# Kernel tuning notes

Measured on AMD Instinct MI355X. Metric: run time of the kernel, lower is better.

Reference implementation:

```python
import jax, jax.numpy as jnp
import numpy as np

B, T, E, H = 2, 1024, 1024, 16
D = E // H
HEAVY_RATIO = 0.1
RECENT_RATIO = 0.1
QUANT_RATIO = 0.5  # module-level global `quantized_ratio`
NEG = jnp.finfo(jnp.float32).min


def setup_inputs() -> dict:
    key = jax.random.key(0)
    ks = jax.random.split(key, 10)
    s = 0.02
    hidden_states = jax.random.normal(ks[0], (B, T, E), jnp.float32)
    causal = jnp.tril(jnp.ones((T, T), bool))
    attention_mask = jnp.broadcast_to(jnp.where(causal, 0.0, NEG).astype(jnp.float32)[None, None], (B, 1, T, T))
    lin = lambda k: (jax.random.normal(k, (E, E), jnp.float32) * s)
    return {
        'hidden_states': hidden_states,
        'attention_mask': attention_mask,
        'Wq': lin(ks[1]), 'bq': jnp.zeros((E,), jnp.float32),
        'Wk': lin(ks[2]), 'bk': jnp.zeros((E,), jnp.float32),
        'Wv': lin(ks[3]), 'bv': jnp.zeros((E,), jnp.float32),
        'Wo': lin(ks[4]), 'bo': jnp.zeros((E,), jnp.float32),
    }


def _heavy_hitter_mask(aw, hb):
    # aw: [BH, T, T] masked attn logits. Faithful to local_heavy_hitter_mask
    # (use_gumbel=False path, no padding). Returns bool mask_bottom [BH, T, T].
    BH, Tt, _ = aw.shape
    tmp = jax.nn.softmax(aw, axis=-1)               # fp32 softmax
    acc = tmp[:, :hb, :].sum(axis=1)                # [BH, T]
    acc = acc * (jnp.arange(Tt) < hb)               # zero cols >= hb
    col_lt_hb = (jnp.arange(Tt) < hb)
    init_block = jnp.broadcast_to(col_lt_hb[None, None, :], (BH, hb, Tt))
    row_ids = jnp.arange(BH)[:, None]
    cols = jnp.arange(Tt)

    def step(acc, xs):
        row, t = xs                                  # row: [BH, T], t: scalar index
        tmp_i = jax.nn.softmax(row, axis=-1)
        _, idx = jax.lax.top_k(acc, hb - 1)          # heavy-hitter indices [BH, hb-1]
        mb = jnp.zeros((BH, Tt), bool).at[row_ids, idx].set(True)
        mb = mb | (cols == t)[None, :]               # always keep current token
        acc = (acc + tmp_i) * mb                     # accumulate + evict
        return acc, mb

    ts = jnp.arange(hb, Tt)
    rows = jnp.swapaxes(aw[:, hb:, :], 0, 1)         # [T-hb, BH, T]
    _, mbs = jax.lax.scan(step, acc, (rows, ts))
    mask = jnp.concatenate([init_block, jnp.swapaxes(mbs, 0, 1)], axis=1)
    return jnp.tril(mask)


def reference(hidden_states, attention_mask, Wq, bq, Wk, bk, Wv, bv, Wo, bo):
    scaling = D ** -0.5
    shape = lambda x: jnp.transpose(x.reshape(B, T, H, D), (0, 2, 1, 3)).reshape(B * H, T, D)
    q = shape((hidden_states @ Wq + bq) * scaling)
    k = shape(hidden_states @ Wk + bk)
    v = shape(hidden_states @ Wv + bv)

    aw = jnp.einsum('btd,bsd->bts', q, k)                      # [BH, T, T]
    aw = aw.reshape(B, H, T, T) + attention_mask               # additive causal mask
    aw = jnp.maximum(aw, NEG).reshape(B * H, T, T)

    hb = int(HEAVY_RATIO * T)
    qt = int(hb * QUANT_RATIO)
    hb = hb + qt                                               # inflated heavy budget
    recent = int(RECENT_RATIO * T)

    mask_bottom = _heavy_hitter_mask(jax.lax.stop_gradient(aw), hb)
    recent_mask = jnp.triu(jnp.ones((T, T), bool), -recent)    # recent window
    mask = jnp.tril(mask_bottom | recent_mask[None])

    # torch code recomputes the identical masked logits; reuse aw
    aw = jnp.where(mask, aw, jnp.min(attention_mask))
    probs = jax.nn.softmax(aw, axis=-1)
    out = jnp.einsum('bts,bsd->btd', probs, v)                 # [BH, T, D]
    out = jnp.transpose(out.reshape(B, H, T, D), (0, 2, 1, 3)).reshape(B, T, E)
    return out @ Wo + bo
```

## Files before the change

### kernel.cpp

```cpp
#include <hip/hip_runtime.h>
#include <hip/hip_bf16.h>
#include <stdint.h>

#define TT 1024
#define EE 1024
#define HH 16
#define DD 64
#define BHN 32
#define HB 153
#define RECW 102
#define RING 16
#define INFLT 8
#define NEGF (-3.4028234663852886e38f)

typedef unsigned long long ull;
typedef __attribute__((ext_vector_type(8))) short bf16x8;
typedef __attribute__((ext_vector_type(4))) float f32x4;

#define OFF_Q  ((size_t)0)
#define OFF_K  (OFF_Q + (size_t)BHN*TT*DD)
#define OFF_V  (OFF_K + (size_t)BHN*TT*DD)
#define OFF_AW (OFF_V + (size_t)BHN*TT*DD)
#define OFF_M  (OFF_AW + (size_t)BHN*TT*TT)
#define OFF_S  (OFF_M + (size_t)BHN*TT)
#define OFF_AO (OFF_S + (size_t)BHN*TT)
#define OFF_END (OFF_AO + (size_t)BHN*TT*DD)

__device__ __forceinline__ ushort f2bf(float x) {
  unsigned u = __float_as_uint(x);
  u = (u + 0x7FFF + ((u >> 16) & 1)) >> 16;
  return (ushort)u;
}
__device__ __forceinline__ float bf2f(ushort h) {
  return __uint_as_float((unsigned)h << 16);
}

__global__ __launch_bounds__(256) void k_pmm(const float* __restrict__ X,
    const float* __restrict__ W, const float* __restrict__ bias,
    float* __restrict__ Y, float scale, int mode) {
  __shared__ ushort Ah[64][72], Al[64][72];
  __shared__ ushort Bh[64][72], Bl[64][72];
  int tid = threadIdx.x, lane = tid & 63, wid = tid >> 6;
  int r = tid >> 2, c0 = (tid & 3) * 16;
  int r0 = blockIdx.y * 64, n0 = blockIdx.x * 64;

  f32x4 acc[4];
  #pragma unroll
  for (int nc = 0; nc < 4; ++nc) acc[nc] = (f32x4){0.f, 0.f, 0.f, 0.f};

  for (int k0 = 0; k0 < EE; k0 += 64) {
    __syncthreads();
    {
      const float4* xs = (const float4*)(X + (size_t)(r0 + r) * EE + k0 + c0);
      #pragma unroll
      for (int q4 = 0; q4 < 4; ++q4) {
        float4 v = xs[q4];
        float f[4] = {v.x, v.y, v.z, v.w};
        ushort hi[4], lo[4];
        #pragma unroll
        for (int u = 0; u < 4; ++u) {
          hi[u] = f2bf(f[u]);
          lo[u] = f2bf(f[u] - bf2f(hi[u]));
        }
        *(unsigned*)&Ah[r][c0 + q4*4]     = (unsigned)hi[0] | ((unsigned)hi[1] << 16);
        *(unsigned*)&Ah[r][c0 + q4*4 + 2] = (unsigned)hi[2] | ((unsigned)hi[3] << 16);
        *(unsigned*)&Al[r][c0 + q4*4]     = (unsigned)lo[0] | ((unsigned)lo[1] << 16);
        *(unsigned*)&Al[r][c0 + q4*4 + 2] = (unsigned)lo[2] | ((unsigned)lo[3] << 16);
      }
    }
    {
      const float4* wsrc = (const float4*)(W + (size_t)(k0 + r) * EE + n0 + c0);
      #pragma unroll
      for (int q4 = 0; q4 < 4; ++q4) {
        float4 v = wsrc[q4];
        float f[4] = {v.x, v.y, v.z, v.w};
        #pragma unroll
        for (int u = 0; u < 4; ++u) {
          ushort hi = f2bf(f[u]);
          ushort lo = f2bf(f[u] - bf2f(hi));
          int c = c0 + q4*4 + u;
          Bh[c][r] = hi;
          Bl[c][r] = lo;
        }
      }
    }
    __syncthreads();
    #pragma unroll
    for (int kb = 0; kb < 2; ++kb) {
      bf16x8 ah = *(const bf16x8*)&Ah[wid*16 + (lane & 15)][kb*32 + (lane >> 4)*8];
      bf16x8 al = *(const bf16x8*)&Al[wid*16 + (lane & 15)][kb*32 + (lane >> 4)*8];
      #pragma unroll
      for (int nc = 0; nc < 4; ++nc) {
        bf16x8 bh_ = *(const bf16x8*)&Bh[nc*16 + (lane & 15)][kb*32 + (lane >> 4)*8];
        bf16x8 bl_ = *(const bf16x8*)&Bl[nc*16 + (lane & 15)][kb*32 + (lane >> 4)*8];
        acc[nc] = __builtin_amdgcn_mfma_f32_16x16x32_bf16(ah, bh_, acc[nc], 0, 0, 0);
        acc[nc] = __builtin_amdgcn_mfma_f32_16x16x32_bf16(al, bh_, acc[nc], 0, 0, 0);
        acc[nc] = __builtin_amdgcn_mfma_f32_16x16x32_bf16(ah, bl_, acc[nc], 0, 0, 0);
      }
    }
  }

  int rowbase = wid*16 + (lane >> 4)*4;
  #pragma unroll
  for (int nc = 0; nc < 4; ++nc) {
    int c = n0 + nc*16 + (lane & 15);
    float bv = bias[c];
    #pragma unroll
    for (int qq = 0; qq < 4; ++qq) {
      int rr = r0 + rowbase + qq;
      float val = (acc[nc][qq] + bv) * scale;
      int b_ = rr >> 10, t_ = rr & 1023, h_ = c >> 6, d_ = c & 63;
      if (mode == 1) {
        Y[(((size_t)(b_*HH + h_) * TT) + t_) * DD + d_] = val;
      } else if (mode == 2) {
        ((ushort*)Y)[(((size_t)(b_*HH + h_) * TT) + t_) * DD + d_] = f2bf(val);
      } else {
        Y[(size_t)rr * EE + c] = val;
      }
    }
  }
}

__global__ __launch_bounds__(256) void k_qk_mfma(const float* __restrict__ q,
    const float* __restrict__ k, float* __restrict__ aw) {
  int bh = blockIdx.y, tt = blockIdx.x;
  int t0 = tt * 64;
  int tid = threadIdx.x, lane = tid & 63, wid = tid >> 6;
  int r = tid >> 2, c0 = (tid & 3) * 16;
  __shared__ ushort Qh[64][72], Ql[64][72];
  __shared__ ushort Kh[64][72], Kl[64][72];
  const float* qb = q + (size_t)bh * TT * DD;
  const float* kb = k + (size_t)bh * TT * DD;
  float* awb = aw + (size_t)bh * TT * TT;

  {
    const float4* xs = (const float4*)(qb + (size_t)(t0 + r) * DD + c0);
    #pragma unroll
    for (int q4 = 0; q4 < 4; ++q4) {
      float4 v = xs[q4];
      float f[4] = {v.x, v.y, v.z, v.w};
      ushort hi[4], lo[4];
      #pragma unroll
      for (int u = 0; u < 4; ++u) {
        hi[u] = f2bf(f[u]);
        lo[u] = f2bf(f[u] - bf2f(hi[u]));
      }
      *(unsigned*)&Qh[r][c0 + q4*4]     = (unsigned)hi[0] | ((unsigned)hi[1] << 16);
      *(unsigned*)&Qh[r][c0 + q4*4 + 2] = (unsigned)hi[2] | ((unsigned)hi[3] << 16);
      *(unsigned*)&Ql[r][c0 + q4*4]     = (unsigned)lo[0] | ((unsigned)lo[1] << 16);
      *(unsigned*)&Ql[r][c0 + q4*4 + 2] = (unsigned)lo[2] | ((unsigned)lo[3] << 16);
    }
  }

  for (int st = 0; st <= tt; ++st) {
    __syncthreads();
    {
      const float4* xs = (const float4*)(kb + (size_t)(st * 64 + r) * DD + c0);
      #pragma unroll
      for (int q4 = 0; q4 < 4; ++q4) {
        float4 v = xs[q4];
        float f[4] = {v.x, v.y, v.z, v.w};
        ushort hi[4], lo[4];
        #pragma unroll
        for (int u = 0; u < 4; ++u) {
          hi[u] = f2bf(f[u]);
          lo[u] = f2bf(f[u] - bf2f(hi[u]));
        }
        *(unsigned*)&Kh[r][c0 + q4*4]     = (unsigned)hi[0] | ((unsigned)hi[1] << 16);
        *(unsigned*)&Kh[r][c0 + q4*4 + 2] = (unsigned)hi[2] | ((unsigned)hi[3] << 16);
        *(unsigned*)&Kl[r][c0 + q4*4]     = (unsigned)lo[0] | ((unsigned)lo[1] << 16);
        *(unsigned*)&Kl[r][c0 + q4*4 + 2] = (unsigned)lo[2] | ((unsigned)lo[3] << 16);
      }
    }
    __syncthreads();
    f32x4 acc[4];
    #pragma unroll
    for (int nc = 0; nc < 4; ++nc) acc[nc] = (f32x4){0.f, 0.f, 0.f, 0.f};
    #pragma unroll
    for (int kb2 = 0; kb2 < 2; ++kb2) {
      bf16x8 ah = *(const bf16x8*)&Qh[wid*16 + (lane & 15)][kb2*32 + (lane >> 4)*8];
      bf16x8 al = *(const bf16x8*)&Ql[wid*16 + (lane & 15)][kb2*32 + (lane >> 4)*8];
      #pragma unroll
      for (int nc = 0; nc < 4; ++nc) {
        bf16x8 bh_ = *(const bf16x8*)&Kh[nc*16 + (lane & 15)][kb2*32 + (lane >> 4)*8];
        bf16x8 bl_ = *(const bf16x8*)&Kl[nc*16 + (lane & 15)][kb2*32 + (lane >> 4)*8];
        acc[nc] = __builtin_amdgcn_mfma_f32_16x16x32_bf16(ah, bh_, acc[nc], 0, 0, 0);
        acc[nc] = __builtin_amdgcn_mfma_f32_16x16x32_bf16(al, bh_, acc[nc], 0, 0, 0);
        acc[nc] = __builtin_amdgcn_mfma_f32_16x16x32_bf16(ah, bl_, acc[nc], 0, 0, 0);
      }
    }
    int rowbase = wid*16 + (lane >> 4)*4;
    #pragma unroll
    for (int nc = 0; nc < 4; ++nc) {
      int s = st * 64 + nc*16 + (lane & 15);
      #pragma unroll
      for (int qq = 0; qq < 4; ++qq) {
        int t_ = t0 + rowbase + qq;
        awb[(size_t)t_ * TT + s] = acc[nc][qq];
      }
    }
  }
}

__global__ __launch_bounds__(256) void k_softmax(float* __restrict__ aw) {
  int bh = blockIdx.y;
  int wid = threadIdx.x >> 6, lane = threadIdx.x & 63;
  int t = blockIdx.x * 4 + wid;
  float* row = aw + ((size_t)bh * TT + t) * TT;
  float vals[16];
  float m = NEGF;
  #pragma unroll
  for (int i = 0; i < 16; ++i) {
    int j = lane + 64*i;
    vals[i] = (j <= t) ? row[j] : NEGF;
    m = fmaxf(m, vals[i]);
  }
  for (int o = 32; o; o >>= 1) m = fmaxf(m, __shfl_xor(m, o));
  float s = 0.f;
  #pragma unroll
  for (int i = 0; i < 16; ++i) {
    int j = lane + 64*i;
    if (j <= t) { vals[i] = expf(vals[i] - m); s += vals[i]; }
  }
  for (int o = 32; o; o >>= 1) s += __shfl_xor(s, o);
  float inv = 1.0f / s;
  #pragma unroll
  for (int i = 0; i < 16; ++i) {
    int j = lane + 64*i;
    if (j <= t) row[j] = vals[i] * inv;
  }
}

__global__ __launch_bounds__(256) void k_init_acc(const float* __restrict__ p,
    float* __restrict__ initacc) {
  int bh = blockIdx.x;
  int c = threadIdx.x;
  float val = 0.f;
  if (c < HB) {
    const float* pb = p + (size_t)bh * TT * TT;
    for (int i = c; i < HB; ++i)
      val += pb[(size_t)i * TT + c];
  }
  initacc[(size_t)bh * 256 + c] = val;
}

#define DPP_HOP(ctrl)                                                        \
  {                                                                          \
    unsigned tt = (unsigned)__builtin_amdgcn_update_dpp(                     \
        (int)0xFFFFFFFFu, (int)x, (ctrl), 0xF, 0xF, false);                  \
    x = x < tt ? x : tt;                                                     \
  }
__device__ __forceinline__ unsigned wave_min_u32(unsigned x) {
  DPP_HOP(0x111)
  DPP_HOP(0x112)
  DPP_HOP(0x114)
  DPP_HOP(0x118)
  DPP_HOP(0x142)
  DPP_HOP(0x143)
  return (unsigned)__builtin_amdgcn_readlane((int)x, 63);
}

__device__ __forceinline__ void gload_lds16(const float* gsrc, float* ldst) {
  __builtin_amdgcn_global_load_lds(
      (const __attribute__((address_space(1))) unsigned int*)gsrc,
      (__attribute__((address_space(3))) unsigned int*)ldst,
      16, 0, 0);
}

__global__ __launch_bounds__(128) void k_scan(const float* __restrict__ p,
    const float* __restrict__ initacc, int* __restrict__ evict_g) {
  int bh = blockIdx.x;
  int tid = threadIdx.x;
  int lane = tid & 63;
  const float* pb = p + (size_t)bh * TT * TT;
  __shared__ float ring[RING][TT];
  __shared__ int ev[TT];
  __shared__ volatile int rdyf[RING];
  __shared__ volatile int donef;
  for (int i = tid; i < TT; i += 128) ev[i] = 0x7fffffff;
  if (tid < RING) rdyf[tid] = -1;
  if (tid == 0) donef = -1;
  __syncthreads();

  if (tid >= 64) {
    #pragma unroll
    for (int r = 0; r < INFLT; ++r) {
      const float* srcrow = pb + (size_t)(HB + r) * TT;
      float* slotbase = ring[(HB + r) & (RING - 1)];
      #pragma unroll
      for (int j = 0; j < 4; ++j)
        gload_lds16(srcrow + j * 256 + lane * 4, slotbase + j * 256);
    }
    for (int r = HB; r < TT; ++r) {
      asm volatile("s_waitcnt vmcnt(28)" ::: "memory");
      if (lane == 0) rdyf[r & (RING - 1)] = r;
      int rn = r + INFLT;
      if (rn - RING >= HB) {
        while (donef < rn - RING) { }
      }
      int rsrc = rn < TT ? rn : TT - 1;
      const float* srcrow = pb + (size_t)rsrc * TT;
      float* slotbase = ring[rn & (RING - 1)];
      #pragma unroll
      for (int j = 0; j < 4; ++j)
        gload_lds16(srcrow + j * 256 + lane * 4, slotbase + j * 256);
    }
  } else {
    bool act2 = lane < (HB - 128);
    int col0 = lane, col1 = 64 + lane, col2 = act2 ? (128 + lane) : 0;
    float sc0 = initacc[(size_t)bh * 256 + lane];
    float sc1 = initacc[(size_t)bh * 256 + 64 + lane];
    float sc2 = act2 ? initacc[(size_t)bh * 256 + 128 + lane] : 0.f;

    while (rdyf[HB & (RING - 1)] != HB) { }
    asm volatile("" ::: "memory");
    int fpeek = rdyf[(HB + 1) & (RING - 1)];
    float r0, r1, r2, rd;
    {
      const float* rb = ring[HB & (RING - 1)];
      r0 = rb[col0]; r1 = rb[col1]; r2 = rb[col2]; rd = rb[HB];
    }
    int cstar;
    {
      unsigned b0 = __float_as_uint(sc0);
      unsigned b1 = __float_as_uint(sc1);
      unsigned b2 = act2 ? __float_as_uint(sc2) : 0xFFFFFFFFu;
      unsigned mn = b0 < b1 ? b0 : b1; mn = mn < b2 ? mn : b2;
      unsigned mstar = wave_min_u32(mn);
      unsigned c0k = (b0 == mstar) ? (unsigned)(1023 - col0) : 0xFFFFFFFFu;
      unsigned c1k = (b1 == mstar) ? (unsigned)(1023 - col1) : 0xFFFFFFFFu;
      unsigned c2k = (act2 && b2 == mstar) ? (unsigned)(1023 - col2) : 0xFFFFFFFFu;
      unsigned cm = c0k < c1k ? c0k : c1k; cm = cm < c2k ? cm : c2k;
      cstar = 1023 - (int)wave_min_u32(cm);
    }

    for (int t = HB; t < TT; ++t) {
      if (col0 == cstar) { ev[col0] = t; col0 = t; sc0 = rd; } else sc0 += r0;
      if (col1 == cstar) { ev[col1] = t; col1 = t; sc1 = rd; } else sc1 += r1;
      if (act2) {
        if (col2 == cstar) { ev[col2] = t; col2 = t; sc2 = rd; } else sc2 += r2;
      }
      if (lane == 0) donef = t;
      if (t + 1 < TT) {
        int slot = (t + 1) & (RING - 1);
        if (fpeek != t + 1) {
          while (rdyf[slot] != t + 1) { }
        }
        asm volatile("" ::: "memory");
        fpeek = rdyf[(t + 2) & (RING - 1)];
        const float* rb = ring[slot];
        r0 = rb[col0]; r1 = rb[col1]; r2 = rb[col2]; rd = rb[t + 1];
        unsigned b0 = __float_as_uint(sc0);
        unsigned b1 = __float_as_uint(sc1);
        unsigned b2 = act2 ? __float_as_uint(sc2) : 0xFFFFFFFFu;
        unsigned mn = b0 < b1 ? b0 : b1; mn = mn < b2 ? mn : b2;
        unsigned mstar = wave_min_u32(mn);
        unsigned c0k = (b0 == mstar) ? (unsigned)(1023 - col0) : 0xFFFFFFFFu;
        unsigned c1k = (b1 == mstar) ? (unsigned)(1023 - col1) : 0xFFFFFFFFu;
        unsigned c2k = (act2 && b2 == mstar) ? (unsigned)(1023 - col2) : 0xFFFFFFFFu;
        unsigned cm = c0k < c1k ? c0k : c1k; cm = cm < c2k ? cm : c2k;
        cstar = 1023 - (int)wave_min_u32(cm);
      }
    }
  }

  __syncthreads();
  int4* dst4 = (int4*)(evict_g + (size_t)bh * TT);
  const int4* src4 = (const int4*)ev;
  for (int i = tid; i < TT/4; i += 128) dst4[i] = src4[i];
}

__global__ __launch_bounds__(256) void k_pv(const float* __restrict__ p,
    const int* __restrict__ evict_g, const ushort* __restrict__ vbf,
    float* __restrict__ ao) {
  int bh = blockIdx.y, tt = blockIdx.x;
  int tid = threadIdx.x, lane = tid & 63, wid = tid >> 6;
  int t0 = tt * 64;
  __shared__ ushort PA[64][72];
  __shared__ ushort VT[64][72];
  __shared__ float rowsum[64];
  __shared__ int et[TT];
  ((int4*)et)[tid] = ((const int4*)(evict_g + (size_t)bh * TT))[tid];
  if (tid < 64) rowsum[tid] = 0.f;
  const float* pb = p + ((size_t)bh * TT + t0) * TT;
  const ushort* vb = vbf + (size_t)bh * TT * DD;

  f32x4 acc[4];
  #pragma unroll
  for (int nc = 0; nc < 4; ++nc) acc[nc] = (f32x4){0.f, 0.f, 0.f, 0.f};

  int r = tid >> 2;
  int c0 = (tid & 3) * 16;
  int tg = t0 + r;
  __syncthreads();

  for (int st = 0; st <= tt; ++st) {
    const float* prow = pb + (size_t)r * TT + st * 64 + c0;
    float part = 0.f;
    ushort tmp16[16];
    #pragma unroll
    for (int q4 = 0; q4 < 4; ++q4) {
      float4 pv4 = *(const float4*)(prow + q4 * 4);
      float vals[4] = {pv4.x, pv4.y, pv4.z, pv4.w};
      #pragma unroll
      for (int u = 0; u < 4; ++u) {
        int j = st * 64 + c0 + q4 * 4 + u;
        bool allow = (j <= tg) && ((et[j] > tg) || (j + RECW >= tg));
        float mv = allow ? vals[u] : 0.f;
        part += mv;
        tmp16[q4 * 4 + u] = f2bf(mv);
      }
    }
    #pragma unroll
    for (int w2 = 0; w2 < 8; ++w2) {
      unsigned pk = (unsigned)tmp16[w2 * 2] | ((unsigned)tmp16[w2 * 2 + 1] << 16);
      *(unsigned*)&PA[r][c0 + w2 * 2] = pk;
    }
    part += __shfl_xor(part, 1);
    part += __shfl_xor(part, 2);
    if ((tid & 3) == 0) rowsum[r] += part;
    {
      const unsigned* vrow32 = (const unsigned*)(vb + (size_t)(st * 64 + r) * DD + c0);
      #pragma unroll
      for (int u = 0; u < 8; ++u) {
        unsigned vv = vrow32[u];
        VT[c0 + u * 2][r] = (ushort)(vv & 0xFFFF);
        VT[c0 + u * 2 + 1][r] = (ushort)(vv >> 16);
      }
    }
    __syncthreads();
    #pragma unroll
    for (int kb = 0; kb < 2; ++kb) {
      bf16x8 af = *(const bf16x8*)&PA[wid * 16 + (lane & 15)][kb * 32 + (lane >> 4) * 8];
      #pragma unroll
      for (int nc = 0; nc < 4; ++nc) {
        bf16x8 bfr = *(const bf16x8*)&VT[nc * 16 + (lane & 15)][kb * 32 + (lane >> 4) * 8];
        acc[nc] = __builtin_amdgcn_mfma_f32_16x16x32_bf16(af, bfr, acc[nc], 0, 0, 0);
      }
    }
    __syncthreads();
  }

  int b_ = bh >> 4, h_ = bh & 15;
  int rl = wid * 16 + (lane >> 4) * 4;
  #pragma unroll
  for (int nc = 0; nc < 4; ++nc) {
    int d = nc * 16 + (lane & 15);
    #pragma unroll
    for (int qq = 0; qq < 4; ++qq) {
      int rr = rl + qq;
      float outv = acc[nc][qq] / rowsum[rr];
      ao[((size_t)b_ * TT + (t0 + rr)) * EE + h_ * DD + d] = outv;
    }
  }
}

extern "C" void kernel_launch(void* const* d_in, const int* in_sizes, int n_in,
                              void* d_out, int out_size, void* d_ws, size_t ws_size,
                              hipStream_t stream) {
  const float* hs = (const float*)d_in[0];
  const float* Wq = (const float*)d_in[2];
  const float* bq = (const float*)d_in[3];
  const float* Wk = (const float*)d_in[4];
  const float* bk = (const float*)d_in[5];
  const float* Wv = (const float*)d_in[6];
  const float* bv = (const float*)d_in[7];
  const float* Wo = (const float*)d_in[8];
  const float* bo = (const float*)d_in[9];
  float* out = (float*)d_out;

  float* ws = (float*)d_ws;
  float* q  = ws + OFF_Q;
  float* k  = ws + OFF_K;
  float* v  = ws + OFF_V;
  float* aw = ws + OFF_AW;
  float* ao = ws + OFF_AO;
  float* initacc = ws + OFF_END;
  int* evict = (int*)(ws + OFF_END + (size_t)BHN * 256);

  dim3 gproj(16, 32);
  k_pmm<<<gproj, 256, 0, stream>>>(hs, Wq, bq, q, 0.125f, 1);
  k_pmm<<<gproj, 256, 0, stream>>>(hs, Wk, bk, k, 1.0f, 1);
  k_pmm<<<gproj, 256, 0, stream>>>(hs, Wv, bv, v, 1.0f, 2);

  dim3 gqk(16, BHN);
  k_qk_mfma<<<gqk, 256, 0, stream>>>(q, k, aw);

  dim3 grs(TT/4, BHN);
  k_softmax<<<grs, 256, 0, stream>>>(aw);

  k_init_acc<<<BHN, 256, 0, stream>>>(aw, initacc);

  k_scan<<<BHN, 128, 0, stream>>>(aw, initacc, evict);

  dim3 gpv(16, BHN);
  k_pv<<<gpv, 256, 0, stream>>>(aw, evict, (const ushort*)v, ao);

  dim3 gout(16, 32);
  k_pmm<<<gout, 256, 0, stream>>>(ao, Wo, bo, out, 1.0f, 0);
}
```

Before: 632.1 us.

## Merge scan producer and consumer waves into one self-prefetching wave

The heavy-hitter scan kernel previously ran a producer wave that streamed rows into an LDS ring and a consumer wave that spun on LDS ready/done flags. Both roles now live in one 64-thread wave. It issues async global-to-LDS loads several rows ahead, waits on vmcnt, and reads with inline ds_read, so all cross-wave spin-wait handshakes are gone. The risk is that the serial eviction loop now also carries load issue and the vmcnt/lgkmcnt waits, which may lengthen each step. Correctness also depends on the hand-tuned vmcnt count and on ordering between LDS writes and later ring reuse.

```diff
diff --git a/kernel.cpp b/kernel.cpp
--- a/kernel.cpp
+++ b/kernel.cpp
@@ -16,6 +16,7 @@
 typedef unsigned long long ull;
 typedef __attribute__((ext_vector_type(8))) short bf16x8;
 typedef __attribute__((ext_vector_type(4))) float f32x4;
+typedef __attribute__((address_space(3))) float lds_float;
 
 #define OFF_Q  ((size_t)0)
 #define OFF_K  (OFF_Q + (size_t)BHN*TT*DD)
@@ -267,37 +268,50 @@
       16, 0, 0);
 }
 
-__global__ __launch_bounds__(128) void k_scan(const float* __restrict__ p,
+__global__ __launch_bounds__(64) void k_scan(const float* __restrict__ p,
     const float* __restrict__ initacc, int* __restrict__ evict_g) {
   int bh = blockIdx.x;
-  int tid = threadIdx.x;
-  int lane = tid & 63;
+  int lane = threadIdx.x;
   const float* pb = p + (size_t)bh * TT * TT;
   __shared__ float ring[RING][TT];
   __shared__ int ev[TT];
-  __shared__ volatile int rdyf[RING];
-  __shared__ volatile int donef;
-  for (int i = tid; i < TT; i += 128) ev[i] = 0x7fffffff;
-  if (tid < RING) rdyf[tid] = -1;
-  if (tid == 0) donef = -1;
-  __syncthreads();
-
-  if (tid >= 64) {
-    #pragma unroll
-    for (int r = 0; r < INFLT; ++r) {
-      const float* srcrow = pb + (size_t)(HB + r) * TT;
-      float* slotbase = ring[(HB + r) & (RING - 1)];
-      #pragma unroll
-      for (int j = 0; j < 4; ++j)
-        gload_lds16(srcrow + j * 256 + lane * 4, slotbase + j * 256);
-    }
-    for (int r = HB; r < TT; ++r) {
-      asm volatile("s_waitcnt vmcnt(28)" ::: "memory");
-      if (lane == 0) rdyf[r & (RING - 1)] = r;
-      int rn = r + INFLT;
-      if (rn - RING >= HB) {
-        while (donef < rn - RING) { }
-      }
+  for (int i = lane; i < TT; i += 64) ev[i] = 0x7fffffff;
+
+  bool act2 = lane < (HB - 128);
+  int col0 = lane, col1 = 64 + lane, col2 = act2 ? (128 + lane) : 0;
+  float sc0 = initacc[(size_t)bh * 256 + lane];
+  float sc1 = initacc[(size_t)bh * 256 + 64 + lane];
+  float sc2 = act2 ? initacc[(size_t)bh * 256 + 128 + lane] : 0.f;
+
+  unsigned ring_base = (unsigned)(size_t)(lds_float*)&ring[0][0];
+
+  #pragma unroll
+  for (int r = 0; r < INFLT; ++r) {
+    const float* srcrow = pb + (size_t)(HB + r) * TT;
+    float* slotbase = ring[(HB + r) & (RING - 1)];
+    #pragma unroll
+    for (int j = 0; j < 4; ++j)
+      gload_lds16(srcrow + j * 256 + lane * 4, slotbase + j * 256);
+  }
+
+  for (int t = HB; t < TT; ++t) {
+    unsigned sbase = ring_base + (unsigned)((t & (RING - 1)) * (TT * 4));
+    unsigned a0 = sbase + (unsigned)col0 * 4;
+    unsigned a1 = sbase + (unsigned)col1 * 4;
+    unsigned a2 = sbase + (unsigned)col2 * 4;
+    unsigned ad = sbase + (unsigned)t * 4;
+    float r0, r1, r2, rd;
+    asm volatile(
+      "s_waitcnt vmcnt(28)\n\t"
+      "ds_read_b32 %0, %4\n\t"
+      "ds_read_b32 %1, %5\n\t"
+      "ds_read_b32 %2, %6\n\t"
+      "ds_read_b32 %3, %7"
+      : "=&v"(r0), "=&v"(r1), "=&v"(r2), "=&v"(rd)
+      : "v"(a0), "v"(a1), "v"(a2), "v"(ad)
+      : "memory");
+    {
+      int rn = t + INFLT;
       int rsrc = rn < TT ? rn : TT - 1;
       const float* srcrow = pb + (size_t)rsrc * TT;
       float* slotbase = ring[rn & (RING - 1)];
@@ -305,69 +319,29 @@
       for (int j = 0; j < 4; ++j)
         gload_lds16(srcrow + j * 256 + lane * 4, slotbase + j * 256);
     }
-  } else {
-    bool act2 = lane < (HB - 128);
-    int col0 = lane, col1 = 64 + lane, col2 = act2 ? (128 + lane) : 0;
-    float sc0 = initacc[(size_t)bh * 256 + lane];
-    float sc1 = initacc[(size_t)bh * 256 + 64 + lane];
-    float sc2 = act2 ? initacc[(size_t)bh * 256 + 128 + lane] : 0.f;
-
-    while (rdyf[HB & (RING - 1)] != HB) { }
-    asm volatile("" ::: "memory");
-    int fpeek = rdyf[(HB + 1) & (RING - 1)];
-    float r0, r1, r2, rd;
-    {
-      const float* rb = ring[HB & (RING - 1)];
-      r0 = rb[col0]; r1 = rb[col1]; r2 = rb[col2]; rd = rb[HB];
-    }
-    int cstar;
-    {
-      unsigned b0 = __float_as_uint(sc0);
-      unsigned b1 = __float_as_uint(sc1);
-      unsigned b2 = act2 ? __float_as_uint(sc2) : 0xFFFFFFFFu;
-      unsigned mn = b0 < b1 ? b0 : b1; mn = mn < b2 ? mn : b2;
-      unsigned mstar = wave_min_u32(mn);
-      unsigned c0k = (b0 == mstar) ? (unsigned)(1023 - col0) : 0xFFFFFFFFu;
-      unsigned c1k = (b1 == mstar) ? (unsigned)(1023 - col1) : 0xFFFFFFFFu;
-      unsigned c2k = (act2 && b2 == mstar) ? (unsigned)(1023 - col2) : 0xFFFFFFFFu;
-      unsigned cm = c0k < c1k ? c0k : c1k; cm = cm < c2k ? cm : c2k;
-      cstar = 1023 - (int)wave_min_u32(cm);
-    }
-
-    for (int t = HB; t < TT; ++t) {
-      if (col0 == cstar) { ev[col0] = t; col0 = t; sc0 = rd; } else sc0 += r0;
-      if (col1 == cstar) { ev[col1] = t; col1 = t; sc1 = rd; } else sc1 += r1;
-      if (act2) {
-        if (col2 == cstar) { ev[col2] = t; col2 = t; sc2 = rd; } else sc2 += r2;
-      }
-      if (lane == 0) donef = t;
-      if (t + 1 < TT) {
-        int slot = (t + 1) & (RING - 1);
-        if (fpeek != t + 1) {
-          while (rdyf[slot] != t + 1) { }
-        }
-        asm volatile("" ::: "memory");
-        fpeek = rdyf[(t + 2) & (RING - 1)];
-        const float* rb = ring[slot];
-        r0 = rb[col0]; r1 = rb[col1]; r2 = rb[col2]; rd = rb[t + 1];
-        unsigned b0 = __float_as_uint(sc0);
-        unsigned b1 = __float_as_uint(sc1);
-        unsigned b2 = act2 ? __float_as_uint(sc2) : 0xFFFFFFFFu;
-        unsigned mn = b0 < b1 ? b0 : b1; mn = mn < b2 ? mn : b2;
-        unsigned mstar = wave_min_u32(mn);
-        unsigned c0k = (b0 == mstar) ? (unsigned)(1023 - col0) : 0xFFFFFFFFu;
-        unsigned c1k = (b1 == mstar) ? (unsigned)(1023 - col1) : 0xFFFFFFFFu;
-        unsigned c2k = (act2 && b2 == mstar) ? (unsigned)(1023 - col2) : 0xFFFFFFFFu;
-        unsigned cm = c0k < c1k ? c0k : c1k; cm = cm < c2k ? cm : c2k;
-        cstar = 1023 - (int)wave_min_u32(cm);
-      }
-    }
-  }
-
-  __syncthreads();
+    unsigned b0 = __float_as_uint(sc0);
+    unsigned b1 = __float_as_uint(sc1);
+    unsigned b2 = act2 ? __float_as_uint(sc2) : 0xFFFFFFFFu;
+    unsigned mn = b0 < b1 ? b0 : b1; mn = mn < b2 ? mn : b2;
+    unsigned mstar = wave_min_u32(mn);
+    unsigned c0k = (b0 == mstar) ? (unsigned)(1023 - col0) : 0xFFFFFFFFu;
+    unsigned c1k = (b1 == mstar) ? (unsigned)(1023 - col1) : 0xFFFFFFFFu;
+    unsigned c2k = (act2 && b2 == mstar) ? (unsigned)(1023 - col2) : 0xFFFFFFFFu;
+    unsigned cm = c0k < c1k ? c0k : c1k; cm = cm < c2k ? cm : c2k;
+    int cstar = 1023 - (int)wave_min_u32(cm);
+    asm volatile("s_waitcnt lgkmcnt(0)" ::: "memory");
+    __builtin_amdgcn_sched_barrier(0);
+    if (col0 == cstar) { ev[col0] = t; col0 = t; sc0 = rd; } else sc0 += r0;
+    if (col1 == cstar) { ev[col1] = t; col1 = t; sc1 = rd; } else sc1 += r1;
+    if (act2) {
+      if (col2 == cstar) { ev[col2] = t; col2 = t; sc2 = rd; } else sc2 += r2;
+    }
+  }
+
   int4* dst4 = (int4*)(evict_g + (size_t)bh * TT);
   const int4* src4 = (const int4*)ev;
-  for (int i = tid; i < TT/4; i += 128) dst4[i] = src4[i];
+  #pragma unroll
+  for (int i = 0; i < 4; ++i) dst4[lane + 64 * i] = src4[lane + 64 * i];
 }
 
 __global__ __launch_bounds__(256) void k_pv(const float* __restrict__ p,
@@ -491,7 +465,7 @@
 
   k_init_acc<<<BHN, 256, 0, stream>>>(aw, initacc);
 
-  k_scan<<<BHN, 128, 0, stream>>>(aw, initacc, evict);
+  k_scan<<<BHN, 64, 0, stream>>>(aw, initacc, evict);
 
   dim3 gpv(16, BHN);
   k_pv<<<gpv, 256, 0, stream>>>(aw, evict, (const ushort*)v, ao);
```

Measured after the change: 590.2 us. 6.6% less time.
